# Kernel tuning notes

Measured on AMD Instinct MI355X. Metric: run time of the kernel, lower is better.

## Reference

```python
import jax, jax.numpy as jnp
import numpy as np

BS, NQ, D = 4, 12500, 256
HEADS, LEVELS, POINTS = 8, 2, 4
HD = D // HEADS
D_FF = 2048
SHAPES = ((100, 100), (50, 50))   # (H, W) per level; sum(H*W) == NQ
STARTS = (0, 10000)


def layer_norm(x, g, b, eps=1e-5):
    m = x.mean(-1, keepdims=True)
    v = ((x - m) ** 2).mean(-1, keepdims=True)
    return (x - m) * jax.lax.rsqrt(v + eps) * g + b


def bilinear_sample(value_l, loc, H, W):
    # value_l: (bs, heads, H*W, hd); loc: (bs, heads, nq, P, 2) normalized [0,1]
    # matches F.grid_sample(align_corners=False, padding_mode='zeros')
    x = loc[..., 0] * W - 0.5
    y = loc[..., 1] * H - 0.5
    x0 = jnp.floor(x)
    y0 = jnp.floor(y)
    wx1 = x - x0
    wy1 = y - y0
    wx0 = 1.0 - wx1
    wy0 = 1.0 - wy1
    x0i = x0.astype(jnp.int32)
    y0i = y0.astype(jnp.int32)

    def gather(xi, yi):
        valid = (xi >= 0) & (xi < W) & (yi >= 0) & (yi < H)
        idx = jnp.clip(yi, 0, H - 1) * W + jnp.clip(xi, 0, W - 1)  # (bs,heads,nq,P)
        b, h, nq, P = idx.shape
        g = jnp.take_along_axis(value_l, idx.reshape(b, h, nq * P, 1), axis=2)
        g = g.reshape(b, h, nq, P, -1)
        return g * valid[..., None].astype(g.dtype)

    g00 = gather(x0i, y0i)
    g10 = gather(x0i + 1, y0i)
    g01 = gather(x0i, y0i + 1)
    g11 = gather(x0i + 1, y0i + 1)
    return (g00 * (wx0 * wy0)[..., None] + g10 * (wx1 * wy0)[..., None]
            + g01 * (wx0 * wy1)[..., None] + g11 * (wx1 * wy1)[..., None])


def setup_inputs() -> dict:
    key = jax.random.key(0)
    ks = jax.random.split(key, 20)
    s = 0.02
    inp = {
        'query': jax.random.normal(ks[0], (BS, NQ, D), jnp.float32),
        'reference_points': jax.random.uniform(ks[1], (BS, NQ, LEVELS, 2), jnp.float32),
        'w_off': s * jax.random.normal(ks[2], (D, HEADS * LEVELS * POINTS * 2), jnp.float32),
        'b_off': s * jax.random.normal(ks[3], (HEADS * LEVELS * POINTS * 2,), jnp.float32),
        'w_attn': s * jax.random.normal(ks[4], (D, HEADS * LEVELS * POINTS), jnp.float32),
        'b_attn': s * jax.random.normal(ks[5], (HEADS * LEVELS * POINTS,), jnp.float32),
        'w_val': s * jax.random.normal(ks[6], (D, D), jnp.float32),
        'b_val': jnp.zeros((D,), jnp.float32),
        'w_out': s * jax.random.normal(ks[7], (D, D), jnp.float32),
        'b_out': jnp.zeros((D,), jnp.float32),
        'w1': s * jax.random.normal(ks[8], (D, D_FF), jnp.float32),
        'b1': jnp.zeros((D_FF,), jnp.float32),
        'w2': s * jax.random.normal(ks[9], (D_FF, D), jnp.float32),
        'b2': jnp.zeros((D,), jnp.float32),
        'ln0_g': jnp.ones((D,), jnp.float32),
        'ln0_b': jnp.zeros((D,), jnp.float32),
        'ln1_g': jnp.ones((D,), jnp.float32),
        'ln1_b': jnp.zeros((D,), jnp.float32),
    }
    return inp


def reference(query, reference_points, w_off, b_off, w_attn, b_attn, w_val, b_val,
              w_out, b_out, w1, b1, w2, b2, ln0_g, ln0_b, ln1_g, ln1_b):
    bs, nq, _ = query.shape
    # value projection; encoder self-attention: value == query tokens
    value = (query @ w_val + b_val).reshape(bs, nq, HEADS, HD).transpose(0, 2, 1, 3)  # (bs,heads,nv,hd)
    off = (query @ w_off + b_off).reshape(bs, nq, HEADS, LEVELS, POINTS, 2)
    aw = (query @ w_attn + b_attn).reshape(bs, nq, HEADS, LEVELS * POINTS)
    aw = jax.nn.softmax(aw, axis=-1).reshape(bs, nq, HEADS, LEVELS, POINTS)

    out = jnp.zeros((bs, HEADS, nq, HD), query.dtype)
    for l, (H, W) in enumerate(SHAPES):
        normalizer = jnp.array([W, H], query.dtype)
        # (bs,nq,heads,P,2)
        loc = reference_points[:, :, None, l, None, :] + off[:, :, :, l] / normalizer
        loc = loc.transpose(0, 2, 1, 3, 4)  # (bs,heads,nq,P,2)
        v_l = value[:, :, STARTS[l]:STARTS[l] + H * W]  # (bs,heads,H*W,hd)
        sampled = bilinear_sample(v_l, loc, H, W)       # (bs,heads,nq,P,hd)
        w_l = aw[:, :, :, l].transpose(0, 2, 1, 3)      # (bs,heads,nq,P)
        out = out + (sampled * w_l[..., None]).sum(axis=3)

    attn_out = out.transpose(0, 2, 1, 3).reshape(bs, nq, D) @ w_out + b_out
    x = layer_norm(query + attn_out, ln0_g, ln0_b)
    h = jax.nn.relu(x @ w1 + b1)
    x = layer_norm(x + (h @ w2 + b2), ln1_g, ln1_b)
    return x
```

## Files before the change

kernel.cpp:

```cpp
#include <hip/hip_runtime.h>


#define NQv 12500
#define BSv 4
#define Dv  256
#define DFF 2048

typedef __attribute__((ext_vector_type(8))) __bf16 bf16x8;
typedef __attribute__((ext_vector_type(4))) float f32x4;

__device__ __forceinline__ ushort f32_to_bf16(float f) {
  unsigned u = __float_as_uint(f);
  u += 0x7FFFu + ((u >> 16) & 1u);
  return (ushort)(u >> 16);
}
__device__ __forceinline__ float bf16_to_f32(ushort u) {
  return __uint_as_float(((unsigned)u) << 16);
}

__global__ __launch_bounds__(256) void conv_bf16_kernel(
    const float* __restrict__ in, ushort* __restrict__ out, int n4) {
  int i = blockIdx.x * 256 + threadIdx.x;
  if (i >= n4) return;
  float4 v = reinterpret_cast<const float4*>(in)[i];
  uint2 st;
  st.x = (unsigned)f32_to_bf16(v.x) | ((unsigned)f32_to_bf16(v.y) << 16);
  st.y = (unsigned)f32_to_bf16(v.z) | ((unsigned)f32_to_bf16(v.w) << 16);
  reinterpret_cast<uint2*>(out)[i] = st;
}

__global__ __launch_bounds__(256) void ttrans_kernel(
    const float* __restrict__ in, ushort* __restrict__ out, int K, int N) {
  __shared__ ushort tl[64][65];
  const int n0 = blockIdx.x * 64, k0 = blockIdx.y * 64;
  const int t = threadIdx.x;
#pragma unroll
  for (int i = 0; i < 16; ++i) {
    int idx = t + 256 * i;
    int r = idx >> 6, c = idx & 63;
    tl[r][c] = f32_to_bf16(in[(size_t)(k0 + r) * N + n0 + c]);
  }
  __syncthreads();
#pragma unroll
  for (int i = 0; i < 16; ++i) {
    int idx = t + 256 * i;
    int r = idx >> 6, c = idx & 63;
    out[(size_t)(n0 + r) * K + k0 + c] = tl[c][r];
  }
}

__global__ __launch_bounds__(256) void build_wcat_kernel(
    const float* __restrict__ w_val, const float* __restrict__ w_off,
    const float* __restrict__ w_attn, const float* __restrict__ b_val,
    const float* __restrict__ b_off, const float* __restrict__ b_attn,
    ushort* __restrict__ wcat, float* __restrict__ bcat) {
  int i = blockIdx.x * 256 + threadIdx.x;
  if (i < 448 * 256) {
    int n = i >> 8, k = i & 255;
    float v = (n < 256) ? w_val[(size_t)k * 256 + n]
              : (n < 384) ? w_off[(size_t)k * 128 + (n - 256)]
                          : w_attn[(size_t)k * 64 + (n - 384)];
    wcat[i] = f32_to_bf16(v);
  }
  if (i < 512)
    bcat[i] = (i < 256) ? b_val[i] : (i < 384) ? b_off[i - 256]
              : (i < 448) ? b_attn[i - 384] : 0.f;
}

template <int MODE>
__global__ __launch_bounds__(256) void stagefmt_kernel(
    const ushort* __restrict__ src, ushort* __restrict__ dst) {
  int i = blockIdx.x * 256 + threadIdx.x;
  int g = i >> 10, c = i & 1023;
  int srcrow, srck;
  if (MODE == 0) { srcrow = (g >> 2) * 128 + (c & 127); srck = (g & 3) * 64 + ((c >> 7) & 7) * 8; }
  if (MODE == 1) { srcrow = c & 255; srck = (g >> 2) * 128 + (g & 3) * 32 + ((c >> 8) & 3) * 8; }
  if (MODE == 2) { srcrow = c & 255; srck = g * 32 + ((c >> 8) & 3) * 8; }
  const int LD = (MODE == 1) ? 2048 : 256;
  *reinterpret_cast<uint4*>(dst + (size_t)i * 8) =
      *reinterpret_cast<const uint4*>(src + (size_t)srcrow * LD + srck);
}

#define TBM 128
#define TBN 128
#define TBK 32

template <int RELU, int NMASK, int SPLIT>
__global__ __launch_bounds__(256) void gemm128_kernel(
    const ushort* __restrict__ A, const ushort* __restrict__ Bt,
    const float* __restrict__ bias, ushort* __restrict__ C,
    ushort* __restrict__ C2,
    int M, int K, int ldc, int Nreal) {
  __shared__ ushort lds[4][TBM * TBK];

  const int t = threadIdx.x;
  const int wid = t >> 6, lane = t & 63;
  const int wr = wid >> 1, wc = wid & 1;
  const int m0 = blockIdx.y * TBM;
  const int n0 = blockIdx.x * TBN;

  int srowA[2], srowB[2], gsl[2];
#pragma unroll
  for (int i = 0; i < 2; i++) {
    int row = i * 64 + (t >> 2);
    int ar = m0 + row;
    srowA[i] = (ar < M) ? ar : (M - 1);
    srowB[i] = n0 + row;
    gsl[i] = ((t & 3) ^ ((row >> 1) & 3)) * 8;
  }

  f32x4 acc[4][4] = {};
  const int nt = K / TBK;
  int cur = 0;

#pragma unroll
  for (int i = 0; i < 2; i++) {
    const int ldsoff = (i * 256 + wid * 64) * 8;
    __builtin_amdgcn_global_load_lds(
        (const __attribute__((address_space(1))) void*)(A + (size_t)srowA[i] * K + gsl[i]),
        (__attribute__((address_space(3))) void*)(lds[0] + ldsoff), 16, 0, 0);
    __builtin_amdgcn_global_load_lds(
        (const __attribute__((address_space(1))) void*)(Bt + (size_t)srowB[i] * K + gsl[i]),
        (__attribute__((address_space(3))) void*)(lds[1] + ldsoff), 16, 0, 0);
  }
  __syncthreads();

  const int rl = lane & 15, kh = lane >> 4;
  for (int tk = 0; tk < nt; ++tk) {
    if (tk + 1 < nt) {
      const int k0 = (tk + 1) * TBK;
      const int nb = (cur ^ 1) * 2;
#pragma unroll
      for (int i = 0; i < 2; i++) {
        const int ldsoff = (i * 256 + wid * 64) * 8;
        __builtin_amdgcn_global_load_lds(
            (const __attribute__((address_space(1))) void*)(A + (size_t)srowA[i] * K + k0 + gsl[i]),
            (__attribute__((address_space(3))) void*)(lds[nb] + ldsoff), 16, 0, 0);
        __builtin_amdgcn_global_load_lds(
            (const __attribute__((address_space(1))) void*)(Bt + (size_t)srowB[i] * K + k0 + gsl[i]),
            (__attribute__((address_space(3))) void*)(lds[nb + 1] + ldsoff), 16, 0, 0);
      }
    }
    {
      const ushort* As = lds[cur * 2];
      const ushort* Bs = lds[cur * 2 + 1];
      bf16x8 afr[4], bfr[4];
#pragma unroll
      for (int ni = 0; ni < 4; ni++) {
        int rowb = wc * 64 + ni * 16 + rl;
        int p = kh ^ ((rowb >> 1) & 3);
        bfr[ni] = *reinterpret_cast<const bf16x8*>(Bs + rowb * 32 + p * 8);
      }
#pragma unroll
      for (int mi = 0; mi < 4; mi++) {
        int rowa = wr * 64 + mi * 16 + rl;
        int p = kh ^ ((rowa >> 1) & 3);
        afr[mi] = *reinterpret_cast<const bf16x8*>(As + rowa * 32 + p * 8);
      }
#pragma unroll
      for (int mi = 0; mi < 4; mi++)
#pragma unroll
        for (int ni = 0; ni < 4; ni++)
          acc[mi][ni] = __builtin_amdgcn_mfma_f32_16x16x32_bf16(afr[mi], bfr[ni], acc[mi][ni], 0, 0, 0);
    }
    __syncthreads();
    cur ^= 1;
  }

  ushort* ldsC = lds[0];
  const int rgrp = lane >> 4, cl = lane & 15;
#pragma unroll
  for (int pass = 0; pass < 2; ++pass) {
    if (wr == pass) {
#pragma unroll
      for (int mi = 0; mi < 4; mi++) {
#pragma unroll
        for (int ni = 0; ni < 4; ni++) {
          int col = wc * 64 + ni * 16 + cl;
          float bv = bias[n0 + col];
#pragma unroll
          for (int r = 0; r < 4; r++) {
            int rloc = mi * 16 + rgrp * 4 + r;
            float v = acc[mi][ni][r] + bv;
            if (RELU) v = fmaxf(v, 0.f);
            ldsC[rloc * 132 + col] = f32_to_bf16(v);
          }
        }
      }
    }
    __syncthreads();
    {
      int rloc = t >> 2;
      int row = m0 + pass * 64 + rloc;
      if (row < M) {
#pragma unroll
        for (int j = 0; j < 4; j++) {
          int col = (t & 3) * 32 + j * 8;
          uint4 v = *reinterpret_cast<const uint4*>(ldsC + rloc * 132 + col);
          if (SPLIT) {
            int gcol = n0 + col;
            if (gcol < 256)
              *reinterpret_cast<uint4*>(C + (size_t)row * 256 + gcol) = v;
            else if (gcol < 448)
              *reinterpret_cast<uint4*>(C2 + (size_t)row * 192 + (gcol - 256)) = v;
          } else if (!NMASK || n0 + col < Nreal) {
            *reinterpret_cast<uint4*>(C + (size_t)row * ldc + n0 + col) = v;
          }
        }
      }
    }
    __syncthreads();
  }
}

__global__ __launch_bounds__(256, 2) void outproj_ln0_kernel(
    const ushort* __restrict__ samp,
    const ushort* __restrict__ wqf,
    const float* __restrict__ bias,
    const float* __restrict__ query,
    const float* __restrict__ g0, const float* __restrict__ be0,
    ushort* __restrict__ xb,
    int M) {
  __shared__ ushort lds_all[32768];
  ushort* As = lds_all;
  ushort* ring0 = lds_all + 16384;

  const int t = threadIdx.x;
  const int wv = t >> 6;
  const int lane = t & 63;
  const int rl = lane & 15, kq = lane >> 4;
  const int cl = lane & 15, g4 = lane >> 4;
  const int m0 = blockIdx.x * 64;

  ushort* ring[2] = {ring0, ring0 + 8192};

  auto issueB = [&](int j, ushort* dst) {
#pragma unroll
    for (int ii = 0; ii < 4; ++ii) {
      int c = t + 256 * ii;
      __builtin_amdgcn_global_load_lds(
          (const __attribute__((address_space(1))) void*)(wqf + (size_t)j * 8192 + (size_t)c * 8),
          (__attribute__((address_space(3))) void*)(dst + (size_t)c * 8), 16, 0, 0);
    }
  };

#pragma unroll
  for (int ii = 0; ii < 8; ++ii) {
    int c = t + 256 * ii;
    __builtin_amdgcn_global_load_lds(
        (const __attribute__((address_space(1))) void*)(
            samp + (size_t)blockIdx.x * 16384 + (size_t)c * 8),
        (__attribute__((address_space(3))) void*)(As + (size_t)c * 8), 16, 0, 0);
  }
  issueB(0, ring[0]);
  __syncthreads();

  f32x4 accF[4][4] = {};
  int cur = 0;

#pragma unroll
  for (int j = 0; j < 8; ++j) {
    if (j + 1 < 8) issueB(j + 1, ring[cur ^ 1]);
    const ushort* Bs = ring[cur];
    bf16x8 afr[4], bfr[4];
#pragma unroll
    for (int mi = 0; mi < 4; mi++)
      afr[mi] = *reinterpret_cast<const bf16x8*>(As + (j * 4 + kq) * 512 + (mi * 16 + rl) * 8);
#pragma unroll
    for (int ni = 0; ni < 4; ni++)
      bfr[ni] = *reinterpret_cast<const bf16x8*>(Bs + kq * 2048 + (wv * 64 + ni * 16 + rl) * 8);
    __builtin_amdgcn_s_setprio(1);
#pragma unroll
    for (int mi = 0; mi < 4; mi++)
#pragma unroll
      for (int ni = 0; ni < 4; ni++)
        accF[mi][ni] = __builtin_amdgcn_mfma_f32_16x16x32_bf16(afr[mi], bfr[ni], accF[mi][ni], 0, 0, 0);
    __builtin_amdgcn_s_setprio(0);
    __syncthreads();
    cur ^= 1;
  }

  float* ptab = (float*)ring0;
  float* mtab = (float*)(ring0 + 2048);

  float bc[4], gc[4], bec[4];
#pragma unroll
  for (int ni = 0; ni < 4; ni++) {
    int col = wv * 64 + ni * 16 + cl;
    bc[ni] = bias[col]; gc[ni] = g0[col]; bec[ni] = be0[col];
  }
#pragma unroll
  for (int mi = 0; mi < 4; mi++) {
#pragma unroll
    for (int ni = 0; ni < 4; ni++) {
      int col = wv * 64 + ni * 16 + cl;
#pragma unroll
      for (int r = 0; r < 4; r++) {
        int row = mi * 16 + g4 * 4 + r;
        int qrow = m0 + row; qrow = (qrow < M) ? qrow : (M - 1);
        accF[mi][ni][r] += bc[ni] + query[(size_t)qrow * 256 + col];
      }
    }
  }
#pragma unroll
  for (int mi = 0; mi < 4; mi++) {
#pragma unroll
    for (int r = 0; r < 4; r++) {
      float s = accF[mi][0][r] + accF[mi][1][r] + accF[mi][2][r] + accF[mi][3][r];
      float sq = accF[mi][0][r] * accF[mi][0][r] + accF[mi][1][r] * accF[mi][1][r] +
                 accF[mi][2][r] * accF[mi][2][r] + accF[mi][3][r] * accF[mi][3][r];
#pragma unroll
      for (int o = 1; o < 16; o <<= 1) {
        s += __shfl_xor(s, o, 64);
        sq += __shfl_xor(sq, o, 64);
      }
      if (cl == 0) {
        int row = mi * 16 + g4 * 4 + r;
        ptab[(row * 4 + wv) * 2 + 0] = s;
        ptab[(row * 4 + wv) * 2 + 1] = sq;
      }
    }
  }
  __syncthreads();
  {
    int row = t >> 2, part = t & 3;
    float s = ptab[(row * 4 + part) * 2 + 0];
    float sq = ptab[(row * 4 + part) * 2 + 1];
    s += __shfl_xor(s, 1, 64);  sq += __shfl_xor(sq, 1, 64);
    s += __shfl_xor(s, 2, 64);  sq += __shfl_xor(sq, 2, 64);
    if (part == 0) {
      float mean = s * (1.f / 256.f);
      float var = sq * (1.f / 256.f) - mean * mean;
      mtab[row * 2 + 0] = mean;
      mtab[row * 2 + 1] = rsqrtf(var + 1e-5f);
    }
  }
  __syncthreads();
#pragma unroll
  for (int mi = 0; mi < 4; mi++) {
#pragma unroll
    for (int r = 0; r < 4; r++) {
      int row = mi * 16 + g4 * 4 + r;
      float2 ms = *reinterpret_cast<const float2*>(mtab + row * 2);
      int grow = m0 + row;
      if (grow < M) {
        size_t base = (size_t)(grow >> 7) * 32768 + (size_t)(grow & 127) * 8;
#pragma unroll
        for (int ni = 0; ni < 4; ni++) {
          int col = wv * 64 + ni * 16 + cl;
          xb[base + (size_t)(col >> 3) * 1024 + (col & 7)] =
              f32_to_bf16((accF[mi][ni][r] - ms.x) * ms.y * gc[ni] + bec[ni]);
        }
      }
    }
  }
}

__global__ __launch_bounds__(512, 1) void ffn_ln_fused_kernel(
    const ushort* __restrict__ xb,
    const ushort* __restrict__ w1f,
    const float* __restrict__ b1,
    const ushort* __restrict__ w2f,
    const float* __restrict__ b2,
    const float* __restrict__ g1, const float* __restrict__ be1,
    float* __restrict__ out, int M) {
  __shared__ ushort lds_all[73856];
  ushort* As = lds_all;
  ushort* Hs = lds_all + 32768;
  ushort* stg0 = lds_all + 49280;

  const int t = threadIdx.x;
  const int wv = t >> 6;
  const int wm = wv >> 2;
  const int wn = wv & 3;
  const int lane = t & 63;
  const int rl = lane & 15, kq = lane >> 4;
  const int cl = lane & 15, g4 = lane >> 4;
  const int m0 = blockIdx.x * 128;

  auto stg = [&](int i) { return stg0 + i * 8192; };

  auto issueB1 = [&](int p, int j, ushort* dst) {
    const ushort* src = w1f + (size_t)(p * 4 + j) * 8192;
#pragma unroll
    for (int ii = 0; ii < 2; ++ii) {
      int c = t + 512 * ii;
      __builtin_amdgcn_global_load_lds(
          (const __attribute__((address_space(1))) void*)(src + (size_t)c * 8),
          (__attribute__((address_space(3))) void*)(dst + (size_t)c * 8), 16, 0, 0);
    }
  };
  auto issueB2 = [&](int p, int tt, ushort* dst) {
    const ushort* src = w2f + (size_t)(p * 4 + tt) * 8192;
#pragma unroll
    for (int ii = 0; ii < 2; ++ii) {
      int c = t + 512 * ii;
      __builtin_amdgcn_global_load_lds(
          (const __attribute__((address_space(1))) void*)(src + (size_t)c * 8),
          (__attribute__((address_space(3))) void*)(dst + (size_t)c * 8), 16, 0, 0);
    }
  };

#pragma unroll
  for (int ii = 0; ii < 8; ++ii) {
    int c = t + 512 * ii;
    __builtin_amdgcn_global_load_lds(
        (const __attribute__((address_space(1))) void*)(
            xb + (size_t)blockIdx.x * 32768 + (size_t)c * 8),
        (__attribute__((address_space(3))) void*)(As + (size_t)c * 8), 16, 0, 0);
  }
  issueB1(0, 0, stg(0));
  issueB1(0, 1, stg(1));
  asm volatile("s_waitcnt vmcnt(2)" ::: "memory");
  __builtin_amdgcn_s_barrier();

  f32x4 acc1[4][2] = {};
  f32x4 accF[4][4] = {};
  int cur = 0;

  for (int p = 0; p < 16; ++p) {
#pragma unroll
    for (int j = 0; j < 8; ++j) {
      int tgt = cur + 2; if (tgt >= 3) tgt -= 3;
      if (j <= 5) {
        const int j2 = j + 2;
        const int p2 = p + (j2 >> 3);
        if ((j2 & 7) < 4) issueB1(p2, j2 & 3, stg(tgt));
        else issueB2(p2, (j2 & 7) - 4, stg(tgt));
        asm volatile("s_waitcnt vmcnt(4) lgkmcnt(0)" ::: "memory");
      } else if (p < 15) {
        const int j2m = (j + 2) & 7;
        issueB1(p + 1, j2m, stg(tgt));
        asm volatile("s_waitcnt vmcnt(4) lgkmcnt(0)" ::: "memory");
      } else if (j == 6) {
        asm volatile("s_waitcnt vmcnt(2) lgkmcnt(0)" ::: "memory");
      } else {
        asm volatile("s_waitcnt vmcnt(0) lgkmcnt(0)" ::: "memory");
      }
      __builtin_amdgcn_s_barrier();
      __builtin_amdgcn_sched_barrier(0);

      const ushort* Bs = stg(cur);
      if (j < 4) {
        __builtin_amdgcn_s_setprio(1);
#pragma unroll
        for (int kk = 0; kk < 2; ++kk) {
          bf16x8 afr[4], bfr[2];
          const int slotA = j * 8 + kk * 4 + kq;
#pragma unroll
          for (int mi = 0; mi < 4; mi++)
            afr[mi] = *reinterpret_cast<const bf16x8*>(
                As + slotA * 1024 + (wm * 64 + mi * 16 + rl) * 8);
          const int slotB = kk * 4 + kq;
#pragma unroll
          for (int ni = 0; ni < 2; ni++)
            bfr[ni] = *reinterpret_cast<const bf16x8*>(
                Bs + slotB * 1024 + (wn * 32 + ni * 16 + rl) * 8);
#pragma unroll
          for (int mi = 0; mi < 4; mi++)
#pragma unroll
            for (int ni = 0; ni < 2; ni++)
              acc1[mi][ni] = __builtin_amdgcn_mfma_f32_16x16x32_bf16(afr[mi], bfr[ni], acc1[mi][ni], 0, 0, 0);
        }
        __builtin_amdgcn_s_setprio(0);
        if (j == 3) {
#pragma unroll
          for (int ni = 0; ni < 2; ni++) {
            int col = wn * 32 + ni * 16 + cl;
            float b1v = b1[p * 128 + col];
            const int s = col >> 3, w8 = col & 7;
#pragma unroll
            for (int mi = 0; mi < 4; mi++) {
#pragma unroll
              for (int r = 0; r < 4; r++) {
                int row = wm * 64 + mi * 16 + g4 * 4 + r;
                Hs[s * 1032 + row * 8 + w8] = f32_to_bf16(fmaxf(acc1[mi][ni][r] + b1v, 0.f));
              }
            }
          }
#pragma unroll
          for (int mi = 0; mi < 4; mi++)
#pragma unroll
            for (int ni = 0; ni < 2; ni++)
              acc1[mi][ni] = (f32x4){0.f, 0.f, 0.f, 0.f};
        }
      } else {
        const int tt = j - 4;
        bf16x8 a2f[4], b2f[4];
#pragma unroll
        for (int mi = 0; mi < 4; mi++)
          a2f[mi] = *reinterpret_cast<const bf16x8*>(
              Hs + (tt * 4 + kq) * 1032 + (wm * 64 + mi * 16 + rl) * 8);
#pragma unroll
        for (int ni = 0; ni < 4; ni++)
          b2f[ni] = *reinterpret_cast<const bf16x8*>(
              Bs + kq * 2048 + (wn * 64 + ni * 16 + rl) * 8);
        __builtin_amdgcn_s_setprio(1);
#pragma unroll
        for (int mi = 0; mi < 4; mi++)
#pragma unroll
          for (int ni = 0; ni < 4; ni++)
            accF[mi][ni] = __builtin_amdgcn_mfma_f32_16x16x32_bf16(a2f[mi], b2f[ni], accF[mi][ni], 0, 0, 0);
        __builtin_amdgcn_s_setprio(0);
      }
      cur = cur + 1; if (cur >= 3) cur -= 3;
    }
  }

  float* ptab = (float*)stg0;
  float* mtab = (float*)(stg0 + 2048);

  float b2c[4], g1c[4], bec[4];
#pragma unroll
  for (int ni = 0; ni < 4; ni++) {
    int col = wn * 64 + ni * 16 + cl;
    b2c[ni] = b2[col]; g1c[ni] = g1[col]; bec[ni] = be1[col];
  }
#pragma unroll
  for (int mi = 0; mi < 4; mi++) {
#pragma unroll
    for (int ni = 0; ni < 4; ni++) {
      int col = wn * 64 + ni * 16 + cl;
#pragma unroll
      for (int r = 0; r < 4; r++) {
        int row = wm * 64 + mi * 16 + g4 * 4 + r;
        ushort xv = As[(col >> 3) * 1024 + row * 8 + (col & 7)];
        accF[mi][ni][r] += b2c[ni] + bf16_to_f32(xv);
      }
    }
  }
#pragma unroll
  for (int mi = 0; mi < 4; mi++) {
#pragma unroll
    for (int r = 0; r < 4; r++) {
      float s = accF[mi][0][r] + accF[mi][1][r] + accF[mi][2][r] + accF[mi][3][r];
      float sq = accF[mi][0][r] * accF[mi][0][r] + accF[mi][1][r] * accF[mi][1][r] +
                 accF[mi][2][r] * accF[mi][2][r] + accF[mi][3][r] * accF[mi][3][r];
#pragma unroll
      for (int o = 1; o < 16; o <<= 1) {
        s += __shfl_xor(s, o, 64);
        sq += __shfl_xor(sq, o, 64);
      }
      if (cl == 0) {
        int row = wm * 64 + mi * 16 + g4 * 4 + r;
        ptab[(row * 4 + wn) * 2 + 0] = s;
        ptab[(row * 4 + wn) * 2 + 1] = sq;
      }
    }
  }
  __syncthreads();
  {
    int row = t >> 2, part = t & 3;
    float s = ptab[(row * 4 + part) * 2 + 0];
    float sq = ptab[(row * 4 + part) * 2 + 1];
    s += __shfl_xor(s, 1, 64);  sq += __shfl_xor(sq, 1, 64);
    s += __shfl_xor(s, 2, 64);  sq += __shfl_xor(sq, 2, 64);
    if (part == 0) {
      float mean = s * (1.f / 256.f);
      float var = sq * (1.f / 256.f) - mean * mean;
      mtab[row * 2 + 0] = mean;
      mtab[row * 2 + 1] = rsqrtf(var + 1e-5f);
    }
  }
  __syncthreads();
#pragma unroll
  for (int mi = 0; mi < 4; mi++) {
#pragma unroll
    for (int r = 0; r < 4; r++) {
      int row = wm * 64 + mi * 16 + g4 * 4 + r;
      float2 ms = *reinterpret_cast<const float2*>(mtab + row * 2);
      int grow = m0 + row;
      if (grow < M) {
#pragma unroll
        for (int ni = 0; ni < 4; ni++) {
          int col = wn * 64 + ni * 16 + cl;
          out[(size_t)grow * 256 + col] = (accF[mi][ni][r] - ms.x) * ms.y * g1c[ni] + bec[ni];
        }
      }
    }
  }
}

__global__ __launch_bounds__(256) void deform_attn_kernel(
    const ushort* __restrict__ val,
    const ushort* __restrict__ oa,
    const float* __restrict__ refp,
    ushort* __restrict__ out,
    int total)
{
  int tid = blockIdx.x * 256 + threadIdx.x;
  if (tid >= total) return;
  int c = tid & 3;
  int idx = tid >> 2;
  int h = idx & 7;
  int row = idx >> 3;
  int bl = row / NQv;

  const ushort* orow = oa + (size_t)row * 192;

  uint lraw = *reinterpret_cast<const uint*>(orow + 128 + h * 8 + c * 2);
  float l0 = bf16_to_f32((ushort)(lraw & 0xffffu));
  float l1 = bf16_to_f32((ushort)(lraw >> 16));
  float mx = fmaxf(l0, l1);
  mx = fmaxf(mx, __shfl_xor(mx, 1, 64));
  mx = fmaxf(mx, __shfl_xor(mx, 2, 64));
  float e0 = __expf(l0 - mx), e1 = __expf(l1 - mx);
  float sm = e0 + e1;
  sm += __shfl_xor(sm, 1, 64);
  sm += __shfl_xor(sm, 2, 64);
  float inv = 1.f / sm;

  ushort o4[4];
  *reinterpret_cast<uint2*>(o4) = *reinterpret_cast<const uint2*>(orow + h * 16 + c * 4);
  float4 rp = *reinterpret_cast<const float4*>(refp + (size_t)row * 4);
  float Wl = (c & 2) ? 50.f : 100.f;
  float fx = ((c & 2) ? rp.z : rp.x) * Wl - 0.5f;
  float fy = ((c & 2) ? rp.w : rp.y) * Wl - 0.5f;
  float myx0 = fx + bf16_to_f32(o4[0]);
  float myy0 = fy + bf16_to_f32(o4[1]);
  float myx1 = fx + bf16_to_f32(o4[2]);
  float myy1 = fy + bf16_to_f32(o4[3]);
  float myw0 = e0 * inv, myw1 = e1 * inv;

  const int lanebase = (threadIdx.x & 63) & ~3;
  float acc8[8] = {};
#pragma unroll
  for (int p = 0; p < 8; ++p) {
    const int src = lanebase | (p >> 1);
    float x = __shfl((p & 1) ? myx1 : myx0, src, 64);
    float y = __shfl((p & 1) ? myy1 : myy0, src, 64);
    float w = __shfl((p & 1) ? myw1 : myw0, src, 64);
    const int W = (p < 4) ? 100 : 50, H = W;
    const ushort* vbase = val + ((size_t)bl * NQv + ((p < 4) ? 0 : 10000)) * 256 + h * 32 + c * 8;
    float x0f = floorf(x), y0f = floorf(y);
    float wx1 = x - x0f, wy1 = y - y0f;
    float wx0 = 1.f - wx1, wy0 = 1.f - wy1;
    int x0 = (int)x0f, y0 = (int)y0f;
    float cw[4] = {w * wx0 * wy0, w * wx1 * wy0, w * wx0 * wy1, w * wx1 * wy1};
    int cx[4] = {x0, x0 + 1, x0, x0 + 1};
    int cy[4] = {y0, y0, y0 + 1, y0 + 1};
#pragma unroll
    for (int cc = 0; cc < 4; cc++) {
      int xi = cx[cc], yi = cy[cc];
      if (xi >= 0 && xi < W && yi >= 0 && yi < H) {
        ushort vr[8];
        *reinterpret_cast<uint4*>(vr) =
            *reinterpret_cast<const uint4*>(vbase + (size_t)(yi * W + xi) * 256);
        float ww = cw[cc];
#pragma unroll
        for (int j = 0; j < 8; j++) acc8[j] += ww * bf16_to_f32(vr[j]);
      }
    }
  }

  ushort st[8];
#pragma unroll
  for (int j = 0; j < 8; j++) st[j] = f32_to_bf16(acc8[j]);
  *reinterpret_cast<uint4*>(out + (size_t)(row >> 6) * 16384 +
                            (size_t)(h * 4 + c) * 512 + (size_t)(row & 63) * 8) =
      *reinterpret_cast<uint4*>(st);
}

extern "C" void kernel_launch(void* const* d_in, const int* in_sizes, int n_in,
                              void* d_out, int out_size, void* d_ws, size_t ws_size,
                              hipStream_t stream) {
  const float* query  = (const float*)d_in[0];
  const float* refp   = (const float*)d_in[1];
  const float* w_off  = (const float*)d_in[2];
  const float* b_off  = (const float*)d_in[3];
  const float* w_attn = (const float*)d_in[4];
  const float* b_attn = (const float*)d_in[5];
  const float* w_val  = (const float*)d_in[6];
  const float* b_val  = (const float*)d_in[7];
  const float* w_out  = (const float*)d_in[8];
  const float* b_out  = (const float*)d_in[9];
  const float* w1     = (const float*)d_in[10];
  const float* b1     = (const float*)d_in[11];
  const float* w2     = (const float*)d_in[12];
  const float* b2     = (const float*)d_in[13];
  const float* ln0g   = (const float*)d_in[14];
  const float* ln0b   = (const float*)d_in[15];
  const float* ln1g   = (const float*)d_in[16];
  const float* ln1b   = (const float*)d_in[17];
  float* outp = (float*)d_out;

  char* ws = (char*)d_ws;
  size_t woff = 0;
  auto walloc = [&](size_t bytes) { size_t r = woff; woff += (bytes + 255) & ~(size_t)255; return r; };
  ushort* wcat = (ushort*)(ws + walloc((size_t)512 * 256 * 2));
  float*  bcat = (float*)(ws + walloc(512 * 4));
  ushort* wqt  = (ushort*)(ws + walloc((size_t)256 * 256 * 2));
  ushort* w1t  = (ushort*)(ws + walloc((size_t)DFF * 256 * 2));
  ushort* w2t  = (ushort*)(ws + walloc((size_t)256 * DFF * 2));
  ushort* wqf  = (ushort*)(ws + walloc((size_t)8 * 8192 * 2));
  ushort* w1f  = (ushort*)(ws + walloc((size_t)64 * 8192 * 2));
  ushort* w2f  = (ushort*)(ws + walloc((size_t)64 * 8192 * 2));
  char* arena = ws + woff;
  size_t arena_sz = (ws_size > woff) ? (ws_size - woff) : 0;

  int nb = ((size_t)BSv * NQv * 1920 + (4u << 20) <= arena_sz) ? BSv : 1;
  const int R = nb * NQv;
  const size_t xbsz = (size_t)((R + 127) / 128) * 65536;
  const size_t smsz = (size_t)((R + 63) / 64) * 32768;
  ushort* qb   = (ushort*)arena;
  ushort* valb = (ushort*)(arena + xbsz);
  ushort* oab  = (ushort*)(arena + xbsz + (size_t)R * 512);
  ushort* samp = (ushort*)(arena + xbsz + (size_t)R * 512 + (size_t)R * 384);
  ushort* xb   = qb;

  build_wcat_kernel<<<dim3(448), dim3(256), 0, stream>>>(
      w_val, w_off, w_attn, b_val, b_off, b_attn, wcat, bcat);
  ttrans_kernel<<<dim3(4, 4), dim3(256), 0, stream>>>(w_out, wqt, Dv, Dv);
  ttrans_kernel<<<dim3(DFF / 64, 4), dim3(256), 0, stream>>>(w1, w1t, Dv, DFF);
  ttrans_kernel<<<dim3(4, DFF / 64), dim3(256), 0, stream>>>(w2, w2t, DFF, Dv);
  stagefmt_kernel<2><<<dim3(32), dim3(256), 0, stream>>>(wqt, wqf);
  stagefmt_kernel<0><<<dim3(256), dim3(256), 0, stream>>>(w1t, w1f);
  stagefmt_kernel<1><<<dim3(256), dim3(256), 0, stream>>>(w2t, w2f);

  const int MT = (R + TBM - 1) / TBM;

  for (int c = 0; c < BSv / nb; c++) {
    const int row0 = c * R;
    const float* qrow = query + (size_t)row0 * Dv;

    conv_bf16_kernel<<<dim3((R * 64 + 255) / 256), dim3(256), 0, stream>>>(qrow, qb, R * 64);

    gemm128_kernel<0, 1, 1><<<dim3(4, MT), dim3(256), 0, stream>>>(
        qb, wcat, bcat, valb, oab, R, Dv, 448, 448);

    deform_attn_kernel<<<dim3((R * 32 + 255) / 256), dim3(256), 0, stream>>>(
        valb, oab, refp + (size_t)row0 * 4, samp, R * 32);

    outproj_ln0_kernel<<<dim3((R + 63) / 64), dim3(256), 0, stream>>>(
        samp, wqf, b_out, qrow, ln0g, ln0b, xb, R);

    ffn_ln_fused_kernel<<<dim3((R + 127) / 128), dim3(512), 0, stream>>>(
        xb, w1f, b1, w2f, b2, ln1g, ln1b, outp + (size_t)row0 * 256, R);
  }
}
```

Baseline: 332.0 us.

## Remap GEMM blocks across XCDs, stage LN0 stores via LDS, remap deform threads

The QKV GEMM now remaps workgroup IDs so that consecutive tiles land on the same XCD, aiming for better L2 locality. The outproj+LN0 epilogue writes bf16 results to LDS first and then issues coalesced 16-byte stores to the tiled xb layout, replacing scattered 2-byte global writes. The deformable attention kernel is re-indexed so adjacent threads handle adjacent query rows for the same head/channel slice, which makes the output stores contiguous. Each thread now computes the full 8-way softmax and loads all offsets itself instead of exchanging them through lane shuffles, trading redundant ALU work and loads for fewer shuffles.

```diff
diff --git a/kernel.cpp b/kernel.cpp
--- a/kernel.cpp
+++ b/kernel.cpp
@@ -96,8 +96,14 @@
   const int t = threadIdx.x;
   const int wid = t >> 6, lane = t & 63;
   const int wr = wid >> 1, wc = wid & 1;
-  const int m0 = blockIdx.y * TBM;
-  const int n0 = blockIdx.x * TBN;
+
+  const int nwg = gridDim.x * gridDim.y;
+  const int lbid = blockIdx.y * gridDim.x + blockIdx.x;
+  const int q = nwg >> 3, r = nwg & 7;
+  const int xcd = lbid & 7, li = lbid >> 3;
+  const int wgid = (xcd < r ? xcd * (q + 1) : r * (q + 1) + (xcd - r) * q) + li;
+  const int m0 = (wgid / gridDim.x) * TBM;
+  const int n0 = (wgid % gridDim.x) * TBN;
 
   int srowA[2], srowB[2], gsl[2];
 #pragma unroll
@@ -342,28 +348,33 @@
     for (int r = 0; r < 4; r++) {
       int row = mi * 16 + g4 * 4 + r;
       float2 ms = *reinterpret_cast<const float2*>(mtab + row * 2);
-      int grow = m0 + row;
-      if (grow < M) {
-        size_t base = (size_t)(grow >> 7) * 32768 + (size_t)(grow & 127) * 8;
-#pragma unroll
-        for (int ni = 0; ni < 4; ni++) {
-          int col = wv * 64 + ni * 16 + cl;
-          xb[base + (size_t)(col >> 3) * 1024 + (col & 7)] =
-              f32_to_bf16((accF[mi][ni][r] - ms.x) * ms.y * gc[ni] + bec[ni]);
-        }
-      }
+#pragma unroll
+      for (int ni = 0; ni < 4; ni++) {
+        int col = wv * 64 + ni * 16 + cl;
+        As[(col >> 3) * 512 + row * 8 + (col & 7)] =
+            f32_to_bf16((accF[mi][ni][r] - ms.x) * ms.y * gc[ni] + bec[ni]);
+      }
+    }
+  }
+  __syncthreads();
+  {
+    const size_t base128 = (size_t)(blockIdx.x >> 1) * 32768 + (size_t)(blockIdx.x & 1) * 512;
+#pragma unroll
+    for (int ii = 0; ii < 8; ++ii) {
+      int c = t + 256 * ii;
+      int s = c >> 6, rl2 = c & 63;
+      if (m0 + rl2 < M)
+        *reinterpret_cast<uint4*>(xb + base128 + (size_t)s * 1024 + (size_t)rl2 * 8) =
+            *reinterpret_cast<const uint4*>(As + (size_t)c * 8);
     }
   }
 }
 
 __global__ __launch_bounds__(512, 1) void ffn_ln_fused_kernel(
-    const ushort* __restrict__ xb,
-    const ushort* __restrict__ w1f,
-    const float* __restrict__ b1,
-    const ushort* __restrict__ w2f,
-    const float* __restrict__ b2,
-    const float* __restrict__ g1, const float* __restrict__ be1,
-    float* __restrict__ out, int M) {
+    const ushort* __restrict__ xb, const ushort* __restrict__ w1f,
+    const float* __restrict__ b1, const ushort* __restrict__ w2f,
+    const float* __restrict__ b2, const float* __restrict__ g1,
+    const float* __restrict__ be1, float* __restrict__ out, int M) {
   __shared__ ushort lds_all[73856];
   ushort* As = lds_all;
   ushort* Hs = lds_all + 32768;
@@ -586,52 +597,46 @@
     const ushort* __restrict__ oa,
     const float* __restrict__ refp,
     ushort* __restrict__ out,
-    int total)
-{
-  int tid = blockIdx.x * 256 + threadIdx.x;
-  if (tid >= total) return;
-  int c = tid & 3;
-  int idx = tid >> 2;
-  int h = idx & 7;
-  int row = idx >> 3;
+    int R) {
+  int g = blockIdx.x * 256 + threadIdx.x;
+  int b64 = g >> 11;
+  int idx = g & 2047;
+  int s = idx >> 6;
+  int rl = idx & 63;
+  int h = s >> 2, c = s & 3;
+  int row = b64 * 64 + rl;
+  if (row >= R) return;
   int bl = row / NQv;
 
   const ushort* orow = oa + (size_t)row * 192;
 
-  uint lraw = *reinterpret_cast<const uint*>(orow + 128 + h * 8 + c * 2);
-  float l0 = bf16_to_f32((ushort)(lraw & 0xffffu));
-  float l1 = bf16_to_f32((ushort)(lraw >> 16));
-  float mx = fmaxf(l0, l1);
-  mx = fmaxf(mx, __shfl_xor(mx, 1, 64));
-  mx = fmaxf(mx, __shfl_xor(mx, 2, 64));
-  float e0 = __expf(l0 - mx), e1 = __expf(l1 - mx);
-  float sm = e0 + e1;
-  sm += __shfl_xor(sm, 1, 64);
-  sm += __shfl_xor(sm, 2, 64);
+  ushort lg[8];
+  *reinterpret_cast<uint4*>(lg) = *reinterpret_cast<const uint4*>(orow + 128 + h * 8);
+  float e[8], mx = -1e30f;
+#pragma unroll
+  for (int i = 0; i < 8; i++) { e[i] = bf16_to_f32(lg[i]); mx = fmaxf(mx, e[i]); }
+  float sm = 0.f;
+#pragma unroll
+  for (int i = 0; i < 8; i++) { e[i] = __expf(e[i] - mx); sm += e[i]; }
   float inv = 1.f / sm;
 
-  ushort o4[4];
-  *reinterpret_cast<uint2*>(o4) = *reinterpret_cast<const uint2*>(orow + h * 16 + c * 4);
+  ushort ofr[16];
+  *reinterpret_cast<uint4*>(ofr)     = *reinterpret_cast<const uint4*>(orow + h * 16);
+  *reinterpret_cast<uint4*>(ofr + 8) = *reinterpret_cast<const uint4*>(orow + h * 16 + 8);
   float4 rp = *reinterpret_cast<const float4*>(refp + (size_t)row * 4);
-  float Wl = (c & 2) ? 50.f : 100.f;
-  float fx = ((c & 2) ? rp.z : rp.x) * Wl - 0.5f;
-  float fy = ((c & 2) ? rp.w : rp.y) * Wl - 0.5f;
-  float myx0 = fx + bf16_to_f32(o4[0]);
-  float myy0 = fy + bf16_to_f32(o4[1]);
-  float myx1 = fx + bf16_to_f32(o4[2]);
-  float myy1 = fy + bf16_to_f32(o4[3]);
-  float myw0 = e0 * inv, myw1 = e1 * inv;
-
-  const int lanebase = (threadIdx.x & 63) & ~3;
+
   float acc8[8] = {};
 #pragma unroll
   for (int p = 0; p < 8; ++p) {
-    const int src = lanebase | (p >> 1);
-    float x = __shfl((p & 1) ? myx1 : myx0, src, 64);
-    float y = __shfl((p & 1) ? myy1 : myy0, src, 64);
-    float w = __shfl((p & 1) ? myw1 : myw0, src, 64);
-    const int W = (p < 4) ? 100 : 50, H = W;
-    const ushort* vbase = val + ((size_t)bl * NQv + ((p < 4) ? 0 : 10000)) * 256 + h * 32 + c * 8;
+    const int l = p >> 2;
+    const float Wl = l ? 50.f : 100.f;
+    const int W = l ? 50 : 100, H = W;
+    float fx = (l ? rp.z : rp.x) * Wl - 0.5f;
+    float fy = (l ? rp.w : rp.y) * Wl - 0.5f;
+    float x = fx + bf16_to_f32(ofr[p * 2 + 0]);
+    float y = fy + bf16_to_f32(ofr[p * 2 + 1]);
+    float w = e[p] * inv;
+    const ushort* vbase = val + ((size_t)bl * NQv + (l ? 10000 : 0)) * 256 + h * 32 + c * 8;
     float x0f = floorf(x), y0f = floorf(y);
     float wx1 = x - x0f, wy1 = y - y0f;
     float wx0 = 1.f - wx1, wy0 = 1.f - wy1;
@@ -656,8 +661,7 @@
   ushort st[8];
 #pragma unroll
   for (int j = 0; j < 8; j++) st[j] = f32_to_bf16(acc8[j]);
-  *reinterpret_cast<uint4*>(out + (size_t)(row >> 6) * 16384 +
-                            (size_t)(h * 4 + c) * 512 + (size_t)(row & 63) * 8) =
+  *reinterpret_cast<uint4*>(out + (size_t)b64 * 16384 + (size_t)s * 512 + (size_t)rl * 8) =
       *reinterpret_cast<uint4*>(st);
 }
 
@@ -701,7 +705,6 @@
   int nb = ((size_t)BSv * NQv * 1920 + (4u << 20) <= arena_sz) ? BSv : 1;
   const int R = nb * NQv;
   const size_t xbsz = (size_t)((R + 127) / 128) * 65536;
-  const size_t smsz = (size_t)((R + 63) / 64) * 32768;
   ushort* qb   = (ushort*)arena;
   ushort* valb = (ushort*)(arena + xbsz);
   ushort* oab  = (ushort*)(arena + xbsz + (size_t)R * 512);
@@ -728,8 +731,8 @@
     gemm128_kernel<0, 1, 1><<<dim3(4, MT), dim3(256), 0, stream>>>(
         qb, wcat, bcat, valb, oab, R, Dv, 448, 448);
 
-    deform_attn_kernel<<<dim3((R * 32 + 255) / 256), dim3(256), 0, stream>>>(
-        valb, oab, refp + (size_t)row0 * 4, samp, R * 32);
+    deform_attn_kernel<<<dim3(((R + 63) / 64) * 8), dim3(256), 0, stream>>>(
+        valb, oab, refp + (size_t)row0 * 4, samp, R);
 
     outproj_ln0_kernel<<<dim3((R + 63) / 64), dim3(256), 0, stream>>>(
         samp, wqf, b_out, qrow, ln0g, ln0b, xb, R);
```

Measured after the change: 415.9 us. 25.3% more time.
